# Kernel tuning notes

Measured on AMD Instinct MI355X. Metric: run time of the kernel, lower is better.

The kernel has to match this reference:

```python
import jax, jax.numpy as jnp
import numpy as np

DIM = 1024
NUM_HEADS = 16
HEAD_DIM = DIM // NUM_HEADS
SCALE = HEAD_DIM ** -0.5


def setup_inputs() -> dict:
    key = jax.random.key(0)
    k_x, k_qw, k_qb, k_pw, k_pb = jax.random.split(key, 5)
    B, N = 4, 4096
    x = jax.random.normal(k_x, (B, N, DIM), dtype=jnp.float32)
    # nn.Linear(dim, 3*dim): weight (out, in), bias (out,)
    s = DIM ** -0.5
    qkv_w = jax.random.uniform(k_qw, (3 * DIM, DIM), jnp.float32, -s, s)
    qkv_b = jax.random.uniform(k_qb, (3 * DIM,), jnp.float32, -s, s)
    proj_w = jax.random.uniform(k_pw, (DIM, DIM), jnp.float32, -s, s)
    proj_b = jax.random.uniform(k_pb, (DIM,), jnp.float32, -s, s)
    return {"x": x, "qkv_w": qkv_w, "qkv_b": qkv_b,
            "proj_w": proj_w, "proj_b": proj_b}


def reference(x, qkv_w, qkv_b, proj_w, proj_b):
    B, N, C = x.shape
    H, D = NUM_HEADS, HEAD_DIM
    # qkv projection: (B,N,3C) -> (B,N,3,H,D)
    qkv = (jnp.einsum('bnc,oc->bno', x, qkv_w) + qkv_b).reshape(B, N, 3, H, D)
    q, k, v = qkv[:, :, 0], qkv[:, :, 1], qkv[:, :, 2]  # each (B,N,H,D)
    # Faithful to source: matmul over the last two dims of (B,N,H,D),
    # i.e. attention scores over the HEAD axis per token -> (B,N,H,H).
    attn = jnp.einsum('bnhd,bngd->bnhg', q, k) * SCALE
    attn = jax.nn.softmax(attn, axis=-1)
    out = jnp.einsum('bnhg,bngd->bnhd', attn, v)      # (B,N,H,D)
    # torch: .transpose(1,2).reshape(B,N,C) -> (B,H,N,D) reshaped to (B,N,C)
    out = out.transpose(0, 2, 1, 3).reshape(B, N, C)
    return jnp.einsum('bnc,oc->bno', out, proj_w) + proj_b
```

## Files before the change

### kernel.cpp

```cpp
#include <hip/hip_runtime.h>
#include <hip/hip_bf16.h>

#define TOK   16384
#define KD    1024
#define NQKV  3072
#define SEQL  4096
#define ATT_SCALE 0.125f

typedef __attribute__((ext_vector_type(4))) float f32x4;
typedef __attribute__((ext_vector_type(8))) short bf16x8;

__device__ __forceinline__ unsigned short f2b(float f){
    union { float f; unsigned u; } x; x.f = f;
    return (unsigned short)((x.u + 0x7FFFu + ((x.u >> 16) & 1u)) >> 16);
}
__device__ __forceinline__ float b2f(unsigned short s){
    union { unsigned u; float f; } x; x.u = ((unsigned)s) << 16;
    return x.f;
}
__device__ __forceinline__ bf16x8 lds8(const unsigned short* p){
    union { uint4 u; bf16x8 v; } t; t.u = *(const uint4*)p; return t.v;
}
__device__ __forceinline__ void glds16(const void* g, void* l){
    __builtin_amdgcn_global_load_lds((const __attribute__((address_space(1))) unsigned*)g,
                                     (__attribute__((address_space(3))) unsigned*)l, 16, 0, 0);
}

__global__ __launch_bounds__(256) void cvt_kernel(const float* __restrict__ in,
                                                  unsigned short* __restrict__ out, int n)
{
    int i = (blockIdx.x * 256 + threadIdx.x) * 8;
    if (i >= n) return;
    float4 a = *(const float4*)(in + i);
    float4 b = *(const float4*)(in + i + 4);
    union { unsigned short u[8]; uint4 v; } t;
    t.u[0]=f2b(a.x); t.u[1]=f2b(a.y); t.u[2]=f2b(a.z); t.u[3]=f2b(a.w);
    t.u[4]=f2b(b.x); t.u[5]=f2b(b.y); t.u[6]=f2b(b.z); t.u[7]=f2b(b.w);
    *(uint4*)(out + i) = t.v;
}

template<bool OUT_BF16>
__global__ __launch_bounds__(512, 2) void gemm256(const unsigned short* __restrict__ A,
        const unsigned short* __restrict__ Bw, const float* __restrict__ bias,
        void* __restrict__ Cp, int Nn)
{
    extern __shared__ unsigned short sm[];
    unsigned short* As = sm;
    unsigned short* Bs = sm + 32768;

    const int tid = threadIdx.x, lane = tid & 63;
    const int w = tid >> 6, wm = w >> 2, wn = w & 3;
    const int rl = lane & 15, kslot = lane >> 4;

    const int gx = gridDim.x;
    const int nwg = gx * gridDim.y;
    int id = blockIdx.y * gx + blockIdx.x;
    id = (id & 7) * (nwg >> 3) + (id >> 3);
    const int cBase = (id % gx) * 256;
    const int mBase = (id / gx) * 256;

    const int srcseg = ((tid & 7) ^ ((tid >> 3) & 7)) * 8;
    const unsigned short* Ag = A  + (size_t)(mBase + (tid >> 3)) * KD + srcseg;
    const unsigned short* Bg = Bw + (size_t)(cBase + (tid >> 3)) * KD + srcseg;

    const int sA = (wm * 128 + rl) * 64;
    const int sB = (wn * 64  + rl) * 64;
    const int xk = rl & 7;
    const int sk0 = (kslot ^ xk) * 8;
    const int sk1 = ((4 + kslot) ^ xk) * 8;

    f32x4 acc[8][4];
    #pragma unroll
    for (int m = 0; m < 8; m++)
        #pragma unroll
        for (int n = 0; n < 4; n++) acc[m][n] = (f32x4)0.f;

#define STAGE_A(bb, kk) { \
        glds16(Ag + (kk),          As + (bb)*16384 + tid*8); \
        glds16(Ag + 64*KD + (kk),  As + (bb)*16384 + 4096  + tid*8); \
        glds16(Ag + 128*KD + (kk), As + (bb)*16384 + 8192  + tid*8); \
        glds16(Ag + 192*KD + (kk), As + (bb)*16384 + 12288 + tid*8); }
#define STAGE_B(bb, kk) { \
        glds16(Bg + (kk),          Bs + (bb)*16384 + tid*8); \
        glds16(Bg + 64*KD + (kk),  Bs + (bb)*16384 + 4096  + tid*8); \
        glds16(Bg + 128*KD + (kk), Bs + (bb)*16384 + 8192  + tid*8); \
        glds16(Bg + 192*KD + (kk), Bs + (bb)*16384 + 12288 + tid*8); }

    STAGE_A(0, 0)
    STAGE_B(0, 0)
    asm volatile("s_waitcnt vmcnt(0)" ::: "memory");
    __builtin_amdgcn_s_barrier();

    bf16x8 af[4][2], bfr[4][2];
    int buf = 0;
    for (int kt = 0; kt < KD; kt += 64) {
        const unsigned short* a = As + buf * 16384;
        const unsigned short* b = Bs + buf * 16384;
        const int nkt = kt + 64;
        #pragma unroll
        for (int m = 0; m < 4; m++) {
            af[m][0] = lds8(a + sA + m * 1024 + sk0);
            af[m][1] = lds8(a + sA + m * 1024 + sk1);
        }
        #pragma unroll
        for (int n = 0; n < 2; n++) {
            bfr[n][0] = lds8(b + sB + n * 1024 + sk0);
            bfr[n][1] = lds8(b + sB + n * 1024 + sk1);
        }
        if (nkt < KD) STAGE_A(buf ^ 1, nkt)
        __builtin_amdgcn_s_barrier();
        asm volatile("s_waitcnt lgkmcnt(0)" ::: "memory");
        __builtin_amdgcn_sched_barrier(0);
        __builtin_amdgcn_s_setprio(1);
        #pragma unroll
        for (int m = 0; m < 4; m++)
            #pragma unroll
            for (int n = 0; n < 2; n++) {
                acc[m][n] = __builtin_amdgcn_mfma_f32_16x16x32_bf16(af[m][0], bfr[n][0], acc[m][n], 0, 0, 0);
                acc[m][n] = __builtin_amdgcn_mfma_f32_16x16x32_bf16(af[m][1], bfr[n][1], acc[m][n], 0, 0, 0);
            }
        __builtin_amdgcn_s_setprio(0);
        __builtin_amdgcn_s_barrier();
        #pragma unroll
        for (int n = 2; n < 4; n++) {
            bfr[n][0] = lds8(b + sB + n * 1024 + sk0);
            bfr[n][1] = lds8(b + sB + n * 1024 + sk1);
        }
        if (nkt < KD) STAGE_B(buf ^ 1, nkt)
        __builtin_amdgcn_s_barrier();
        asm volatile("s_waitcnt lgkmcnt(0)" ::: "memory");
        __builtin_amdgcn_sched_barrier(0);
        __builtin_amdgcn_s_setprio(1);
        #pragma unroll
        for (int m = 0; m < 4; m++)
            #pragma unroll
            for (int n = 2; n < 4; n++) {
                acc[m][n] = __builtin_amdgcn_mfma_f32_16x16x32_bf16(af[m][0], bfr[n][0], acc[m][n], 0, 0, 0);
                acc[m][n] = __builtin_amdgcn_mfma_f32_16x16x32_bf16(af[m][1], bfr[n][1], acc[m][n], 0, 0, 0);
            }
        __builtin_amdgcn_s_setprio(0);
        __builtin_amdgcn_s_barrier();
        #pragma unroll
        for (int m = 0; m < 4; m++) {
            af[m][0] = lds8(a + sA + (m + 4) * 1024 + sk0);
            af[m][1] = lds8(a + sA + (m + 4) * 1024 + sk1);
        }
        __builtin_amdgcn_s_barrier();
        asm volatile("s_waitcnt lgkmcnt(0)" ::: "memory");
        __builtin_amdgcn_sched_barrier(0);
        __builtin_amdgcn_s_setprio(1);
        #pragma unroll
        for (int m = 0; m < 4; m++)
            #pragma unroll
            for (int n = 0; n < 2; n++) {
                acc[4 + m][n] = __builtin_amdgcn_mfma_f32_16x16x32_bf16(af[m][0], bfr[n][0], acc[4 + m][n], 0, 0, 0);
                acc[4 + m][n] = __builtin_amdgcn_mfma_f32_16x16x32_bf16(af[m][1], bfr[n][1], acc[4 + m][n], 0, 0, 0);
            }
        __builtin_amdgcn_s_setprio(0);
        __builtin_amdgcn_s_barrier();
        __builtin_amdgcn_s_setprio(1);
        #pragma unroll
        for (int m = 0; m < 4; m++)
            #pragma unroll
            for (int n = 2; n < 4; n++) {
                acc[4 + m][n] = __builtin_amdgcn_mfma_f32_16x16x32_bf16(af[m][0], bfr[n][0], acc[4 + m][n], 0, 0, 0);
                acc[4 + m][n] = __builtin_amdgcn_mfma_f32_16x16x32_bf16(af[m][1], bfr[n][1], acc[4 + m][n], 0, 0, 0);
            }
        __builtin_amdgcn_s_setprio(0);
        asm volatile("s_waitcnt vmcnt(0)" ::: "memory");
        __builtin_amdgcn_s_barrier();
        buf ^= 1;
    }
#undef STAGE_A
#undef STAGE_B

    #pragma unroll
    for (int n = 0; n < 4; n++) {
        const int col = cBase + wn * 64 + n * 16 + rl;
        const float bv = bias[col];
        #pragma unroll
        for (int m = 0; m < 8; m++) {
            const int row0 = mBase + wm * 128 + m * 16 + kslot * 4;
            #pragma unroll
            for (int i = 0; i < 4; i++) {
                const float val = acc[m][n][i] + bv;
                if (OUT_BF16) ((unsigned short*)Cp)[(size_t)(row0 + i) * Nn + col] = f2b(val);
                else          ((float*)Cp)[(size_t)(row0 + i) * Nn + col] = val;
            }
        }
    }
}

__global__ __launch_bounds__(256) void attn_kernel(const unsigned short* __restrict__ qkv,
                                                   unsigned short* __restrict__ outp)
{
    __shared__ __align__(16) unsigned short qs[4][48 * 72];
    __shared__ float ps[4][16 * 17];
    const int tid = threadIdx.x, w = tid >> 6, lane = tid & 63;
    const int t = blockIdx.x * 4 + w;

    const unsigned short* src = qkv + (size_t)t * NQKV;
    #pragma unroll
    for (int i = 0; i < 6; i++) {
        const int e = i * 512 + lane * 8;
        uint4 v = *(const uint4*)(src + e);
        *(uint4*)&qs[w][(e >> 6) * 72 + (e & 63)] = v;
    }
    __syncthreads();

    const int h = lane & 15, g0 = lane >> 4;
    uint4 qv[8];
    #pragma unroll
    for (int i = 0; i < 8; i++) qv[i] = *(const uint4*)&qs[w][h * 72 + i * 8];
    float s[4];
    #pragma unroll
    for (int i = 0; i < 4; i++) {
        const int g = g0 * 4 + i;
        float a = 0.f;
        #pragma unroll
        for (int c = 0; c < 8; c++) {
            uint4 kv = *(const uint4*)&qs[w][(16 + g) * 72 + c * 8];
            uint qa[4] = {qv[c].x, qv[c].y, qv[c].z, qv[c].w};
            uint ka[4] = {kv.x, kv.y, kv.z, kv.w};
            #pragma unroll
            for (int u = 0; u < 4; u++) {
                a += b2f((unsigned short)qa[u]) * b2f((unsigned short)ka[u]);
                a += b2f((unsigned short)(qa[u] >> 16)) * b2f((unsigned short)(ka[u] >> 16));
            }
        }
        s[i] = a * ATT_SCALE;
    }
    float mx = fmaxf(fmaxf(s[0], s[1]), fmaxf(s[2], s[3]));
    mx = fmaxf(mx, __shfl_xor(mx, 16, 64));
    mx = fmaxf(mx, __shfl_xor(mx, 32, 64));
    float p[4], smv = 0.f;
    #pragma unroll
    for (int i = 0; i < 4; i++) { p[i] = __expf(s[i] - mx); smv += p[i]; }
    smv += __shfl_xor(smv, 16, 64);
    smv += __shfl_xor(smv, 32, 64);
    const float inv = 1.f / smv;
    #pragma unroll
    for (int i = 0; i < 4; i++) ps[w][h * 17 + g0 * 4 + i] = p[i] * inv;
    __syncthreads();

    const int h2 = lane >> 2, db = (lane & 3) * 16;
    float pr[16];
    #pragma unroll
    for (int g = 0; g < 16; g++) pr[g] = ps[w][h2 * 17 + g];
    float acc[16];
    #pragma unroll
    for (int j = 0; j < 16; j++) acc[j] = 0.f;
    #pragma unroll
    for (int g = 0; g < 16; g++) {
        const unsigned short* vp = &qs[w][(32 + g) * 72 + db];
        uint4 v0 = *(const uint4*)vp;
        uint4 v1 = *(const uint4*)(vp + 8);
        const float pg = pr[g];
        uint va[8] = {v0.x, v0.y, v0.z, v0.w, v1.x, v1.y, v1.z, v1.w};
        #pragma unroll
        for (int u = 0; u < 8; u++) {
            acc[2*u]   += pg * b2f((unsigned short)va[u]);
            acc[2*u+1] += pg * b2f((unsigned short)(va[u] >> 16));
        }
    }
    const int b = t >> 12, n = t & 4095;
    const int n1 = h2 * 256 + (n >> 4);
    const int c0 = (n & 15) * 64 + db;
    union { unsigned short u[16]; uint4 v[2]; } st;
    #pragma unroll
    for (int j = 0; j < 16; j++) st.u[j] = f2b(acc[j]);
    unsigned short* dst = outp + ((size_t)(b * SEQL + n1)) * 1024 + c0;
    *(uint4*)dst       = st.v[0];
    *(uint4*)(dst + 8) = st.v[1];
}

extern "C" void kernel_launch(void* const* d_in, const int* in_sizes, int n_in,
                              void* d_out, int out_size, void* d_ws, size_t ws_size,
                              hipStream_t stream)
{
    const float* x      = (const float*)d_in[0];
    const float* qkv_w  = (const float*)d_in[1];
    const float* qkv_b  = (const float*)d_in[2];
    const float* proj_w = (const float*)d_in[3];
    const float* proj_b = (const float*)d_in[4];

    unsigned short* xb  = (unsigned short*)d_ws;
    unsigned short* qkv = xb + (size_t)TOK * KD;
    unsigned short* qwb = qkv + (size_t)TOK * NQKV;
    unsigned short* pwb = qwb + (size_t)NQKV * KD;
    unsigned short* att = xb;

    hipFuncSetAttribute(reinterpret_cast<const void*>(&gemm256<true>),
                        hipFuncAttributeMaxDynamicSharedMemorySize, 131072);
    hipFuncSetAttribute(reinterpret_cast<const void*>(&gemm256<false>),
                        hipFuncAttributeMaxDynamicSharedMemorySize, 131072);

    cvt_kernel<<<dim3(TOK * KD / 2048), dim3(256), 0, stream>>>(x, xb, TOK * KD);
    cvt_kernel<<<dim3(NQKV * KD / 2048), dim3(256), 0, stream>>>(qkv_w, qwb, NQKV * KD);
    cvt_kernel<<<dim3(KD * KD / 2048), dim3(256), 0, stream>>>(proj_w, pwb, KD * KD);

    gemm256<true><<<dim3(NQKV / 256, TOK / 256), dim3(512), 131072, stream>>>(
        xb, qwb, qkv_b, qkv, NQKV);
    attn_kernel<<<dim3(TOK / 4), dim3(256), 0, stream>>>(qkv, att);
    gemm256<false><<<dim3(KD / 256, TOK / 256), dim3(512), 131072, stream>>>(
        att, pwb, proj_b, (float*)d_out, KD);
}
```

Measured before the change: 215.6 us.

## Restructure GEMM mainloop into 4-stage BK=32 pipeline with single sync per step

Replaces the double-buffered BK=64 GEMM mainloop, which used four barrier-separated MFMA phases, with a 4-buffer ring of BK=32 tiles. Each step prefetches two tiles ahead, waits on a partial vmcnt, reads all A/B fragments at once and then issues 32 MFMAs in one block. The aim is to keep more global loads in flight and to cut the number of barriers and interleaved phases per K step. LDS use stays the same, and the XOR swizzle is narrowed to 4 segments to fit the 32-wide rows. The risks are more loop iterations, hand-counted vmcnt values that must stay correct, and possible bank conflicts with the narrower swizzle.

Result: slower. 228.2 us (+5.8%).

```diff
diff --git a/kernel.cpp b/kernel.cpp
--- a/kernel.cpp
+++ b/kernel.cpp
@@ -59,15 +59,14 @@
     const int cBase = (id % gx) * 256;
     const int mBase = (id / gx) * 256;
 
-    const int srcseg = ((tid & 7) ^ ((tid >> 3) & 7)) * 8;
-    const unsigned short* Ag = A  + (size_t)(mBase + (tid >> 3)) * KD + srcseg;
-    const unsigned short* Bg = Bw + (size_t)(cBase + (tid >> 3)) * KD + srcseg;
-
-    const int sA = (wm * 128 + rl) * 64;
-    const int sB = (wn * 64  + rl) * 64;
-    const int xk = rl & 7;
-    const int sk0 = (kslot ^ xk) * 8;
-    const int sk1 = ((4 + kslot) ^ xk) * 8;
+    const int srow = tid >> 2;
+    const int sseg = ((tid & 3) ^ ((tid >> 2) & 3)) * 8;
+    const unsigned short* Ag = A  + (size_t)(mBase + srow) * KD + sseg;
+    const unsigned short* Bg = Bw + (size_t)(cBase + srow) * KD + sseg;
+
+    const int psg = (kslot ^ (rl & 3)) * 8;
+    const int aoff = (wm * 128 + rl) * 32 + psg;
+    const int boff = (wn * 64  + rl) * 32 + psg;
 
     f32x4 acc[8][4];
     #pragma unroll
@@ -75,117 +74,75 @@
         #pragma unroll
         for (int n = 0; n < 4; n++) acc[m][n] = (f32x4)0.f;
 
-#define STAGE_A(bb, kk) { \
-        glds16(Ag + (kk),          As + (bb)*16384 + tid*8); \
-        glds16(Ag + 64*KD + (kk),  As + (bb)*16384 + 4096  + tid*8); \
-        glds16(Ag + 128*KD + (kk), As + (bb)*16384 + 8192  + tid*8); \
-        glds16(Ag + 192*KD + (kk), As + (bb)*16384 + 12288 + tid*8); }
-#define STAGE_B(bb, kk) { \
-        glds16(Bg + (kk),          Bs + (bb)*16384 + tid*8); \
-        glds16(Bg + 64*KD + (kk),  Bs + (bb)*16384 + 4096  + tid*8); \
-        glds16(Bg + 128*KD + (kk), Bs + (bb)*16384 + 8192  + tid*8); \
-        glds16(Bg + 192*KD + (kk), Bs + (bb)*16384 + 12288 + tid*8); }
-
-    STAGE_A(0, 0)
-    STAGE_B(0, 0)
-    asm volatile("s_waitcnt vmcnt(0)" ::: "memory");
-    __builtin_amdgcn_s_barrier();
-
-    bf16x8 af[4][2], bfr[4][2];
-    int buf = 0;
-    for (int kt = 0; kt < KD; kt += 64) {
-        const unsigned short* a = As + buf * 16384;
-        const unsigned short* b = Bs + buf * 16384;
-        const int nkt = kt + 64;
-        #pragma unroll
-        for (int m = 0; m < 4; m++) {
-            af[m][0] = lds8(a + sA + m * 1024 + sk0);
-            af[m][1] = lds8(a + sA + m * 1024 + sk1);
-        }
-        #pragma unroll
-        for (int n = 0; n < 2; n++) {
-            bfr[n][0] = lds8(b + sB + n * 1024 + sk0);
-            bfr[n][1] = lds8(b + sB + n * 1024 + sk1);
-        }
-        if (nkt < KD) STAGE_A(buf ^ 1, nkt)
+#define STAGE(bb, kk) { \
+        glds16(Ag + (kk),            As + (bb)*8192 + tid*8); \
+        glds16(Ag + 128*KD + (kk),   As + (bb)*8192 + 4096 + tid*8); \
+        glds16(Bg + (kk),            Bs + (bb)*8192 + tid*8); \
+        glds16(Bg + 128*KD + (kk),   Bs + (bb)*8192 + 4096 + tid*8); }
+
+#define DSREAD(bb) { \
+        const unsigned short* a_ = As + (bb)*8192; \
+        const unsigned short* b_ = Bs + (bb)*8192; \
+        _Pragma("unroll") \
+        for (int m = 0; m < 8; m++) af[m] = lds8(a_ + aoff + m * 512); \
+        _Pragma("unroll") \
+        for (int n = 0; n < 4; n++) bf[n] = lds8(b_ + boff + n * 512); }
+
+#define MFMA32() { \
+        __builtin_amdgcn_s_setprio(1); \
+        _Pragma("unroll") \
+        for (int m = 0; m < 8; m++) \
+            _Pragma("unroll") \
+            for (int n = 0; n < 4; n++) \
+                acc[m][n] = __builtin_amdgcn_mfma_f32_16x16x32_bf16(af[m], bf[n], acc[m][n], 0, 0, 0); \
+        __builtin_amdgcn_s_setprio(0); }
+
+    bf16x8 af[8], bf[4];
+
+    STAGE(0, 0)
+    STAGE(1, 32)
+
+    for (int t = 0; t < 30; ++t) {
+        STAGE((t + 2) & 3, (t + 2) * 32)
+        asm volatile("s_waitcnt vmcnt(8)" ::: "memory");
+        __builtin_amdgcn_s_barrier();
+        DSREAD(t & 3)
         __builtin_amdgcn_s_barrier();
         asm volatile("s_waitcnt lgkmcnt(0)" ::: "memory");
         __builtin_amdgcn_sched_barrier(0);
-        __builtin_amdgcn_s_setprio(1);
-        #pragma unroll
-        for (int m = 0; m < 4; m++)
+        MFMA32()
+    }
+    asm volatile("s_waitcnt vmcnt(4)" ::: "memory");
+    __builtin_amdgcn_s_barrier();
+    DSREAD(2)
+    __builtin_amdgcn_s_barrier();
+    asm volatile("s_waitcnt lgkmcnt(0)" ::: "memory");
+    __builtin_amdgcn_sched_barrier(0);
+    MFMA32()
+    asm volatile("s_waitcnt vmcnt(0)" ::: "memory");
+    __builtin_amdgcn_s_barrier();
+    DSREAD(3)
+    asm volatile("s_waitcnt lgkmcnt(0)" ::: "memory");
+    __builtin_amdgcn_sched_barrier(0);
+    MFMA32()
+#undef STAGE
+#undef DSREAD
+#undef MFMA32
+
+    float bv[4];
+    #pragma unroll
+    for (int n = 0; n < 4; n++) bv[n] = bias[cBase + wn * 64 + n * 16 + rl];
+    #pragma unroll
+    for (int m = 0; m < 8; m++) {
+        #pragma unroll
+        for (int i = 0; i < 4; i++) {
+            const size_t row = mBase + wm * 128 + m * 16 + kslot * 4 + i;
             #pragma unroll
-            for (int n = 0; n < 2; n++) {
-                acc[m][n] = __builtin_amdgcn_mfma_f32_16x16x32_bf16(af[m][0], bfr[n][0], acc[m][n], 0, 0, 0);
-                acc[m][n] = __builtin_amdgcn_mfma_f32_16x16x32_bf16(af[m][1], bfr[n][1], acc[m][n], 0, 0, 0);
-            }
-        __builtin_amdgcn_s_setprio(0);
-        __builtin_amdgcn_s_barrier();
-        #pragma unroll
-        for (int n = 2; n < 4; n++) {
-            bfr[n][0] = lds8(b + sB + n * 1024 + sk0);
-            bfr[n][1] = lds8(b + sB + n * 1024 + sk1);
-        }
-        if (nkt < KD) STAGE_B(buf ^ 1, nkt)
-        __builtin_amdgcn_s_barrier();
-        asm volatile("s_waitcnt lgkmcnt(0)" ::: "memory");
-        __builtin_amdgcn_sched_barrier(0);
-        __builtin_amdgcn_s_setprio(1);
-        #pragma unroll
-        for (int m = 0; m < 4; m++)
-            #pragma unroll
-            for (int n = 2; n < 4; n++) {
-                acc[m][n] = __builtin_amdgcn_mfma_f32_16x16x32_bf16(af[m][0], bfr[n][0], acc[m][n], 0, 0, 0);
-                acc[m][n] = __builtin_amdgcn_mfma_f32_16x16x32_bf16(af[m][1], bfr[n][1], acc[m][n], 0, 0, 0);
-            }
-        __builtin_amdgcn_s_setprio(0);
-        __builtin_amdgcn_s_barrier();
-        #pragma unroll
-        for (int m = 0; m < 4; m++) {
-            af[m][0] = lds8(a + sA + (m + 4) * 1024 + sk0);
-            af[m][1] = lds8(a + sA + (m + 4) * 1024 + sk1);
-        }
-        __builtin_amdgcn_s_barrier();
-        asm volatile("s_waitcnt lgkmcnt(0)" ::: "memory");
-        __builtin_amdgcn_sched_barrier(0);
-        __builtin_amdgcn_s_setprio(1);
-        #pragma unroll
-        for (int m = 0; m < 4; m++)
-            #pragma unroll
-            for (int n = 0; n < 2; n++) {
-                acc[4 + m][n] = __builtin_amdgcn_mfma_f32_16x16x32_bf16(af[m][0], bfr[n][0], acc[4 + m][n], 0, 0, 0);
-                acc[4 + m][n] = __builtin_amdgcn_mfma_f32_16x16x32_bf16(af[m][1], bfr[n][1], acc[4 + m][n], 0, 0, 0);
-            }
-        __builtin_amdgcn_s_setprio(0);
-        __builtin_amdgcn_s_barrier();
-        __builtin_amdgcn_s_setprio(1);
-        #pragma unroll
-        for (int m = 0; m < 4; m++)
-            #pragma unroll
-            for (int n = 2; n < 4; n++) {
-                acc[4 + m][n] = __builtin_amdgcn_mfma_f32_16x16x32_bf16(af[m][0], bfr[n][0], acc[4 + m][n], 0, 0, 0);
-                acc[4 + m][n] = __builtin_amdgcn_mfma_f32_16x16x32_bf16(af[m][1], bfr[n][1], acc[4 + m][n], 0, 0, 0);
-            }
-        __builtin_amdgcn_s_setprio(0);
-        asm volatile("s_waitcnt vmcnt(0)" ::: "memory");
-        __builtin_amdgcn_s_barrier();
-        buf ^= 1;
-    }
-#undef STAGE_A
-#undef STAGE_B
-
-    #pragma unroll
-    for (int n = 0; n < 4; n++) {
-        const int col = cBase + wn * 64 + n * 16 + rl;
-        const float bv = bias[col];
-        #pragma unroll
-        for (int m = 0; m < 8; m++) {
-            const int row0 = mBase + wm * 128 + m * 16 + kslot * 4;
-            #pragma unroll
-            for (int i = 0; i < 4; i++) {
-                const float val = acc[m][n][i] + bv;
-                if (OUT_BF16) ((unsigned short*)Cp)[(size_t)(row0 + i) * Nn + col] = f2b(val);
-                else          ((float*)Cp)[(size_t)(row0 + i) * Nn + col] = val;
+            for (int n = 0; n < 4; n++) {
+                const int col = cBase + wn * 64 + n * 16 + rl;
+                const float val = acc[m][n][i] + bv[n];
+                if (OUT_BF16) ((unsigned short*)Cp)[row * Nn + col] = f2b(val);
+                else          ((float*)Cp)[row * Nn + col] = val;
             }
         }
     }
```
